# Kernel tuning notes

Hardware: AMD Instinct MI355X
Metric: run time of the kernel (lower is better)

Reference implementation:

```python
import jax, jax.numpy as jnp
import numpy as np

H = 16      # num_attention_heads
D = 64      # attention_head_size
HID = H * D # hidden_size = 1024
N = 1024    # seq_len == max_len
K = 1024    # position_buckets == att_span (K >= N so un-clamped indices stay in range)
EPS = 1e-7  # layer_norm_eps


def setup_inputs() -> dict:
    key = jax.random.key(0)
    ks = jax.random.split(key, 12)

    def w(k, shape):
        return jax.random.normal(k, shape, dtype=jnp.float32) * 0.02

    return {
        "hidden_states": jax.random.normal(ks[0], (1, N, HID), dtype=jnp.float32),
        "rel_embeddings": jax.random.normal(ks[1], (2 * K, HID), dtype=jnp.float32),
        "Wq": w(ks[2], (HID, HID)), "bq": jnp.zeros((HID,), jnp.float32),
        "Wk": w(ks[3], (HID, HID)), "bk": jnp.zeros((HID,), jnp.float32),
        "Wv": w(ks[4], (HID, HID)), "bv": jnp.zeros((HID,), jnp.float32),
        "Wpk": w(ks[5], (HID, HID)), "bpk": jnp.zeros((HID,), jnp.float32),
        "Wpq": w(ks[6], (HID, HID)), "bpq": jnp.zeros((HID,), jnp.float32),
        "Wo": w(ks[7], (HID, HID)), "bo": jnp.zeros((HID,), jnp.float32),
        "ln_g": jnp.ones((HID,), jnp.float32),
        "ln_b": jnp.zeros((HID,), jnp.float32),
    }


def _heads(x):
    # (L, HID) -> (H, L, D)   (batch size is 1, matching the baked-in id offsets)
    L = x.shape[0]
    return x.reshape(L, H, D).transpose(1, 0, 2)


def reference(hidden_states, rel_embeddings, Wq, bq, Wk, bk, Wv, bv,
              Wpk, bpk, Wpq, bpq, Wo, bo, ln_g, ln_b):
    hs = hidden_states[0]                       # (N, HID)
    q = _heads(hs @ Wq.T + bq)                  # (H, N, D)
    k = _heads(hs @ Wk.T + bk)                  # (H, N, D)
    v = _heads(hs @ Wv.T + bv)                  # (H, N, D)

    scale = jnp.sqrt(jnp.asarray(D * 3, jnp.float32))  # scale_factor = 1 + c2p + p2c = 3
    scores = jnp.einsum('hid,hjd->hij', q, k) / scale  # (H, N, N)

    pos_k = _heads(rel_embeddings @ Wpk.T + bpk)       # (H, 2K, D)
    pos_q = _heads(rel_embeddings @ Wpq.T + bpq)       # (H, 2K, D)

    rows = jnp.arange(N)[:, None]                      # (N, 1)
    # ids[i, j] = (i - j) + K  (no clamp in the original; valid since K >= N)
    idx = K + jnp.arange(N)[:, None] - jnp.arange(N)[None, :]  # (N, N)

    # c2p: gather c2p_att[h, i, K + i - j]
    c2p_att = jnp.einsum('hid,hkd->hik', q, pos_k)     # (H, N, 2K)
    c2p = c2p_att[:, rows, idx]                        # (H, N, N)

    # p2c: gather p2c_att[h, i, K + j - i], then transpose last two dims
    p2c_att = jnp.einsum('hid,hkd->hik', k, pos_q)     # (H, N, 2K)
    p2c = jnp.swapaxes(p2c_att[:, rows, idx.T], -1, -2)  # (H, N, N)

    scores = scores + (c2p + p2c) / scale
    attn = jax.nn.softmax(scores, axis=-1)             # (H, N, N)

    ctx = jnp.einsum('hij,hjd->hid', attn, v)          # (H, N, D)
    ctx = ctx.transpose(1, 0, 2).reshape(1, N, HID)    # (1, N, HID)

    # DebertaV2SelfOutput: dense + residual LayerNorm
    out = ctx @ Wo.T + bo
    x = out + hidden_states
    mu = jnp.mean(x, axis=-1, keepdims=True)
    var = jnp.mean(jnp.square(x - mu), axis=-1, keepdims=True)
    return ((x - mu) / jnp.sqrt(var + EPS)) * ln_g + ln_b
```

## Files before the change

### kernel.cpp

```cpp
#include <hip/hip_runtime.h>
#include <stdint.h>

#define HID 1024
#define NSEQ 1024
#define KREL 1024
#define NHEAD 16
#define DHEAD 64

typedef __attribute__((ext_vector_type(8))) short bhalf8;
typedef __attribute__((ext_vector_type(4))) float floatx4;

__device__ inline uint16_t f2bf(float f) {
  union { float f; uint32_t u; } c; c.f = f;
  uint32_t u = c.u;
  return (uint16_t)((u + 0x7fffu + ((u >> 16) & 1u)) >> 16);
}
__device__ inline uint32_t pkbf(float a, float b) {
  union { float f; uint32_t u; } x, y; x.f = a; y.f = b;
#if __has_builtin(__builtin_amdgcn_perm)
  return __builtin_amdgcn_perm(x.u + 0x8000u, y.u + 0x8000u, 0x03020706u);
#else
  return ((x.u + 0x8000u) >> 16) | ((y.u + 0x8000u) & 0xffff0000u);
#endif
}
__device__ inline uint32_t cvtpk(float lo, float hi) {
  uint32_t r;
  asm("v_cvt_pk_bf16_f32 %0, %1, %2" : "=v"(r) : "v"(lo), "v"(hi));
  return r;
}
__device__ inline uint4 cvt8(float4 a, float4 b) {
  uint4 r;
  r.x = cvtpk(a.x, a.y); r.y = cvtpk(a.z, a.w);
  r.z = cvtpk(b.x, b.y); r.w = cvtpk(b.z, b.w);
  return r;
}

struct ProjArgs {
  const float* A[5];
  const float* W[5];
  const float* bias[5];
  uint16_t* C[5];
  int trans[5];
};
__global__ __launch_bounds__(512) void proj_gemm(ProjArgs pa) {
  __shared__ uint16_t a_s[2][128 * 40];
  __shared__ uint16_t b_s[2][128 * 40];
  int bidx = blockIdx.x;
  int xcd = bidx & 7, idx = bidx >> 3;
  int g = xcd * 7 + (idx >> 3);
  int nt = idx & 7;
  int z, mt;
  if (g < 24) { z = g >> 3; mt = g & 7; }
  else { int g2 = g - 24; z = 3 + (g2 >> 4); mt = g2 & 15; }
  const float* A = pa.A[z];
  const float* W = pa.W[z];
  int i0 = mt * 128, n0 = nt * 128;

  int t = threadIdx.x;
  int lane = t & 63, w = t >> 6;
  int fm = lane & 15, kq = lane >> 4;
  int wm = (w >> 2) * 64, wn = (w & 3) * 32;

  int ra = t >> 2, ca = (t & 3) * 8;
  const float* Ap = A + (size_t)(i0 + ra) * HID + ca;
  const float* Wp = W + (size_t)(n0 + ra) * HID + ca;

  floatx4 acc[4][2] = {};

  float4 fa0 = *(const float4*)(Ap);
  float4 fa1 = *(const float4*)(Ap + 4);
  float4 fb0 = *(const float4*)(Wp);
  float4 fb1 = *(const float4*)(Wp + 4);
  *(uint4*)(&a_s[0][ra * 40 + ca]) = cvt8(fa0, fa1);
  *(uint4*)(&b_s[0][ra * 40 + ca]) = cvt8(fb0, fb1);

  for (int kt = 0; kt < 32; ++kt) {
    __syncthreads();
    int cur = kt & 1;
    if (kt < 31) {
      int ko = (kt + 1) * 32;
      fa0 = *(const float4*)(Ap + ko);
      fa1 = *(const float4*)(Ap + ko + 4);
      fb0 = *(const float4*)(Wp + ko);
      fb1 = *(const float4*)(Wp + ko + 4);
    }
    const uint16_t* as = &a_s[cur][0];
    const uint16_t* bs = &b_s[cur][0];
    bhalf8 af[4], bf[2];
#pragma unroll
    for (int m2 = 0; m2 < 4; ++m2)
      af[m2] = *(bhalf8*)(as + (wm + m2 * 16 + fm) * 40 + kq * 8);
#pragma unroll
    for (int n2 = 0; n2 < 2; ++n2)
      bf[n2] = *(bhalf8*)(bs + (wn + n2 * 16 + fm) * 40 + kq * 8);
#pragma unroll
    for (int m2 = 0; m2 < 4; ++m2)
#pragma unroll
      for (int n2 = 0; n2 < 2; ++n2)
        acc[m2][n2] = __builtin_amdgcn_mfma_f32_16x16x32_bf16(af[m2], bf[n2], acc[m2][n2], 0, 0, 0);
    if (kt < 31) {
      int nxt = cur ^ 1;
      *(uint4*)(&a_s[nxt][ra * 40 + ca]) = cvt8(fa0, fa1);
      *(uint4*)(&b_s[nxt][ra * 40 + ca]) = cvt8(fb0, fb1);
    }
  }

  const float* bias = pa.bias[z];
  uint16_t* C = pa.C[z];
  int tr = pa.trans[z];
#pragma unroll
  for (int m2 = 0; m2 < 4; ++m2) {
    int rowb = i0 + wm + m2 * 16 + kq * 4;
#pragma unroll
    for (int n2 = 0; n2 < 2; ++n2) {
      int col = n0 + wn + n2 * 16 + fm;
      float bv = bias[col];
      floatx4 v = acc[m2][n2];
      if (tr) {
        uint2 p = { pkbf(v[0] + bv, v[1] + bv), pkbf(v[2] + bv, v[3] + bv) };
        *(uint2*)(C + (size_t)col * NSEQ + rowb) = p;
      } else {
#pragma unroll
        for (int r = 0; r < 4; ++r)
          C[(size_t)(rowb + r) * HID + col] = f2bf(v[r] + bv);
      }
    }
  }
}

__global__ __launch_bounds__(256) void out_gemm(const uint16_t* __restrict__ Abf,
                                                const float* __restrict__ W,
                                                const float* __restrict__ bias,
                                                float* __restrict__ C) {
  __shared__ uint16_t a_s[2][64 * 40];
  __shared__ uint16_t b_s[2][64 * 40];
  int bidx = blockIdx.x;
  int i0 = (bidx >> 4) * 64, n0 = (bidx & 15) * 64;
  int t = threadIdx.x;
  int lane = t & 63, w = t >> 6;
  int fm = lane & 15, kq = lane >> 4;
  int wm = (w >> 1) * 32, wn = (w & 1) * 32;
  int ra = t >> 2, ca = (t & 3) * 8;
  const uint16_t* Ap = Abf + (size_t)(i0 + ra) * HID + ca;
  const float* Wp = W + (size_t)(n0 + ra) * HID + ca;
  floatx4 acc00 = {0,0,0,0}, acc01 = {0,0,0,0}, acc10 = {0,0,0,0}, acc11 = {0,0,0,0};
  uint4 ua = *(const uint4*)(Ap);
  float4 fw0 = *(const float4*)(Wp);
  float4 fw1 = *(const float4*)(Wp + 4);
  *(uint4*)(&a_s[0][ra * 40 + ca]) = ua;
  *(uint4*)(&b_s[0][ra * 40 + ca]) = cvt8(fw0, fw1);
  for (int kt = 0; kt < 32; ++kt) {
    __syncthreads();
    int cur = kt & 1;
    if (kt < 31) {
      int ko = (kt + 1) * 32;
      ua = *(const uint4*)(Ap + ko);
      fw0 = *(const float4*)(Wp + ko);
      fw1 = *(const float4*)(Wp + ko + 4);
    }
    const uint16_t* as = &a_s[cur][0];
    const uint16_t* bs = &b_s[cur][0];
    bhalf8 a0 = *(bhalf8*)(as + (wm + fm) * 40 + kq * 8);
    bhalf8 a1 = *(bhalf8*)(as + (wm + 16 + fm) * 40 + kq * 8);
    bhalf8 b0 = *(bhalf8*)(bs + (wn + fm) * 40 + kq * 8);
    bhalf8 b1 = *(bhalf8*)(bs + (wn + 16 + fm) * 40 + kq * 8);
    acc00 = __builtin_amdgcn_mfma_f32_16x16x32_bf16(a0, b0, acc00, 0, 0, 0);
    acc01 = __builtin_amdgcn_mfma_f32_16x16x32_bf16(a0, b1, acc01, 0, 0, 0);
    acc10 = __builtin_amdgcn_mfma_f32_16x16x32_bf16(a1, b0, acc10, 0, 0, 0);
    acc11 = __builtin_amdgcn_mfma_f32_16x16x32_bf16(a1, b1, acc11, 0, 0, 0);
    if (kt < 31) {
      int nxt = cur ^ 1;
      *(uint4*)(&a_s[nxt][ra * 40 + ca]) = ua;
      *(uint4*)(&b_s[nxt][ra * 40 + ca]) = cvt8(fw0, fw1);
    }
  }
  int rb0 = kq * 4;
#define EPO(ACC, SM, SN)                                                   \
  {                                                                        \
    int rowb = i0 + wm + (SM)*16 + rb0;                                    \
    int col = n0 + wn + (SN)*16 + fm;                                      \
    float bv_ = bias[col];                                                 \
    _Pragma("unroll")                                                      \
    for (int rr = 0; rr < 4; ++rr)                                         \
      C[(size_t)(rowb + rr) * HID + col] = ACC[rr] + bv_;                  \
  }
  EPO(acc00, 0, 0) EPO(acc01, 0, 1) EPO(acc10, 1, 0) EPO(acc11, 1, 1)
#undef EPO
}

__global__ __launch_bounds__(256) void attn_kernel(const uint16_t* __restrict__ qg,
                                                   const uint16_t* __restrict__ kg,
                                                   const uint16_t* __restrict__ vtg,
                                                   const uint16_t* __restrict__ pkg,
                                                   const uint16_t* __restrict__ pqg,
                                                   uint16_t* __restrict__ ctx) {
  const float RSCALE = 0.07216878364870323f;
  __shared__ uint16_t Qs[32][72];
  __shared__ uint16_t Ks[32][72];
  __shared__ uint16_t Vt[64][40];
  __shared__ float C2Ps[2][32][68];
  __shared__ float P2C[2][32][68];
  __shared__ float Sqk[2][32][36];
  __shared__ uint16_t Pbf[32][40];
  __shared__ float m_sm[32], l_sm[32], al_sm[32];

  int t = threadIdx.x;
  int lane = t & 63, w = t >> 6;
  int fm = lane & 15;
  int kq = lane >> 4;

  int b = blockIdx.x;
  int xcd = b & 7, slot = b >> 3;
  int h = xcd * 2 + (slot & 1);
  int i0 = (slot >> 1) * 32;
  int cb = h * DHEAD;

  {
    int r = t >> 3, chq = (t & 7) * 8;
    *(uint4*)(&Qs[r][chq]) = *(const uint4*)(qg + (size_t)(i0 + r) * HID + cb + chq);
  }
  if (t < 32) { m_sm[t] = -1e30f; l_sm[t] = 0.f; }

  floatx4 opv0 = {0,0,0,0}, opv1 = {0,0,0,0};
  int wn = w * 16;
  int smt = w >> 1, snt = w & 1;
  int i2 = t >> 3, jj4 = (t & 7) * 4;

  int pr = t >> 3, pch = (t & 7) * 8;
  int rV = t >> 2, cV = (t & 3) * 8;
  const uint16_t* kb = kg + cb + pch;
  const uint16_t* vb = vtg + (size_t)(cb + rV) * HID + cV;

  int ntb = (w & 1) * 2;
  int brow_f = ntb * 16 + fm;
  const uint16_t* bgp = ((w < 2) ? pkg : pqg) + cb + kq * 8;
  int cbase = 31 - brow_f + kq * 4;

  uint4 rk, rv;
  bhalf8 nbA0, nbA1, nbB0, nbB1;

#define STAGE1(BUF, BA0, BA1, BB0, BB1)                                          \
  do {                                                                           \
    if (w < 2) {                                                                 \
      _Pragma("unroll")                                                          \
      for (int mt = 0; mt < 2; ++mt) {                                           \
        bhalf8 a0 = *(bhalf8*)(&Qs[mt * 16 + fm][kq * 8]);                       \
        bhalf8 a1 = *(bhalf8*)(&Qs[mt * 16 + fm][kq * 8 + 32]);                  \
        floatx4 ac0 = {0,0,0,0}, ac1 = {0,0,0,0};                                \
        ac0 = __builtin_amdgcn_mfma_f32_16x16x32_bf16(a0, BA0, ac0, 0, 0, 0);    \
        ac0 = __builtin_amdgcn_mfma_f32_16x16x32_bf16(a1, BA1, ac0, 0, 0, 0);    \
        ac1 = __builtin_amdgcn_mfma_f32_16x16x32_bf16(a0, BB0, ac1, 0, 0, 0);    \
        ac1 = __builtin_amdgcn_mfma_f32_16x16x32_bf16(a1, BB1, ac1, 0, 0, 0);    \
        _Pragma("unroll")                                                        \
        for (int r = 0; r < 4; ++r) {                                            \
          int i = mt * 16 + kq * 4 + r;                                          \
          C2Ps[BUF][i][(cbase + mt * 16 + r) & 63] = ac0[r];                     \
          C2Ps[BUF][i][(cbase + mt * 16 + r - 16) & 63] = ac1[r];                \
        }                                                                        \
      }                                                                          \
    } else {                                                                     \
      _Pragma("unroll")                                                          \
      for (int mt = 0; mt < 2; ++mt) {                                           \
        bhalf8 a0 = *(bhalf8*)(&Ks[mt * 16 + fm][kq * 8]);                       \
        bhalf8 a1 = *(bhalf8*)(&Ks[mt * 16 + fm][kq * 8 + 32]);                  \
        floatx4 ac0 = {0,0,0,0}, ac1 = {0,0,0,0};                                \
        ac0 = __builtin_amdgcn_mfma_f32_16x16x32_bf16(a0, BA0, ac0, 0, 0, 0);    \
        ac0 = __builtin_amdgcn_mfma_f32_16x16x32_bf16(a1, BA1, ac0, 0, 0, 0);    \
        ac1 = __builtin_amdgcn_mfma_f32_16x16x32_bf16(a0, BB0, ac1, 0, 0, 0);    \
        ac1 = __builtin_amdgcn_mfma_f32_16x16x32_bf16(a1, BB1, ac1, 0, 0, 0);    \
        _Pragma("unroll")                                                        \
        for (int r = 0; r < 4; ++r) {                                            \
          int jr = mt * 16 + kq * 4 + r;                                         \
          P2C[BUF][jr][brow_f] = ac0[r];                                         \
          P2C[BUF][jr][brow_f + 16] = ac1[r];                                    \
        }                                                                        \
      }                                                                          \
    }                                                                            \
    {                                                                            \
      bhalf8 qa0 = *(bhalf8*)(&Qs[smt * 16 + fm][kq * 8]);                       \
      bhalf8 qa1 = *(bhalf8*)(&Qs[smt * 16 + fm][kq * 8 + 32]);                  \
      bhalf8 kb0 = *(bhalf8*)(&Ks[snt * 16 + fm][kq * 8]);                       \
      bhalf8 kb1 = *(bhalf8*)(&Ks[snt * 16 + fm][kq * 8 + 32]);                  \
      floatx4 sacc = {0,0,0,0};                                                  \
      sacc = __builtin_amdgcn_mfma_f32_16x16x32_bf16(qa0, kb0, sacc, 0, 0, 0);   \
      sacc = __builtin_amdgcn_mfma_f32_16x16x32_bf16(qa1, kb1, sacc, 0, 0, 0);   \
      _Pragma("unroll")                                                          \
      for (int r = 0; r < 4; ++r)                                                \
        Sqk[BUF][smt * 16 + kq * 4 + r][snt * 16 + fm] = sacc[r];                \
    }                                                                            \
  } while (0)

  rk = *(const uint4*)(kb);
  rv = *(const uint4*)(vb);
  *(uint4*)(&Ks[pr][pch]) = rk;
  *(uint4*)(&Vt[rV][cV]) = rv;
  __syncthreads();
  rk = *(const uint4*)(kb + (size_t)(32 + pr) * HID);
  rv = *(const uint4*)(vb + 32);
  {
    int rbase = KREL + i0 - 31;
    int r0 = rbase + brow_f;      if (r0 > 2047) r0 = 2047;
    int r1 = rbase + brow_f + 16; if (r1 > 2047) r1 = 2047;
    bhalf8 tA0 = *(const bhalf8*)(bgp + ((size_t)r0 << 10));
    bhalf8 tA1 = *(const bhalf8*)(bgp + ((size_t)r0 << 10) + 32);
    bhalf8 tB0 = *(const bhalf8*)(bgp + ((size_t)r1 << 10));
    bhalf8 tB1 = *(const bhalf8*)(bgp + ((size_t)r1 << 10) + 32);
    STAGE1(0, tA0, tA1, tB0, tB1);
  }
  __syncthreads();
  {
    *(uint4*)(&Ks[pr][pch]) = rk;
    rk = *(const uint4*)(kb + (size_t)(64 + pr) * HID);
    int rb1 = KREL + i0 - 63;
    int r0 = rb1 + brow_f;
    nbA0 = *(const bhalf8*)(bgp + ((size_t)r0 << 10));
    nbA1 = *(const bhalf8*)(bgp + ((size_t)r0 << 10) + 32);
    nbB0 = *(const bhalf8*)(bgp + ((size_t)(r0 + 16) << 10));
    nbB1 = *(const bhalf8*)(bgp + ((size_t)(r0 + 16) << 10) + 32);
  }
  __syncthreads();

  for (int jt = 0; jt < NSEQ / 32; ++jt) {
    int cur = jt & 1;

    float4 v_sqk = *(const float4*)(&Sqk[cur][i2][jj4]);
    float4 v_c2p = *(const float4*)(&C2Ps[cur][i2][jj4]);
    float p0 = P2C[cur][jj4 + 0][i2 - jj4 + 31];
    float p1 = P2C[cur][jj4 + 1][i2 - jj4 + 30];
    float p2 = P2C[cur][jj4 + 2][i2 - jj4 + 29];
    float p3 = P2C[cur][jj4 + 3][i2 - jj4 + 28];

    if (jt < 31) {
      int bi = cur ^ 1;
      STAGE1(bi, nbA0, nbA1, nbB0, nbB1);
    }

    {
      float sv0 = (v_sqk.x + v_c2p.x + p0) * RSCALE;
      float sv1 = (v_sqk.y + v_c2p.y + p1) * RSCALE;
      float sv2 = (v_sqk.z + v_c2p.z + p2) * RSCALE;
      float sv3 = (v_sqk.w + v_c2p.w + p3) * RSCALE;
      float mx = fmaxf(fmaxf(sv0, sv1), fmaxf(sv2, sv3));
      mx = fmaxf(mx, __shfl_xor(mx, 1));
      mx = fmaxf(mx, __shfl_xor(mx, 2));
      mx = fmaxf(mx, __shfl_xor(mx, 4));
      float m_old = m_sm[i2];
      float m_new = fmaxf(m_old, mx);
      float al = __expf(m_old - m_new);
      float e0 = __expf(sv0 - m_new);
      float e1 = __expf(sv1 - m_new);
      float e2 = __expf(sv2 - m_new);
      float e3 = __expf(sv3 - m_new);
      uint2 pk2v;
      pk2v.x = (uint32_t)f2bf(e0) | ((uint32_t)f2bf(e1) << 16);
      pk2v.y = (uint32_t)f2bf(e2) | ((uint32_t)f2bf(e3) << 16);
      *(uint2*)(&Pbf[i2][jj4]) = pk2v;
      float ts = (e0 + e1) + (e2 + e3);
      ts += __shfl_xor(ts, 1);
      ts += __shfl_xor(ts, 2);
      ts += __shfl_xor(ts, 4);
      if (jj4 == 0) { m_sm[i2] = m_new; l_sm[i2] = l_sm[i2] * al + ts; al_sm[i2] = al; }
    }
    __syncthreads();

    {
      floatx4 al0 = *(const floatx4*)(&al_sm[kq * 4]);
      floatx4 al1 = *(const floatx4*)(&al_sm[16 + kq * 4]);
#pragma unroll
      for (int r = 0; r < 4; ++r) {
        opv0[r] *= al0[r];
        opv1[r] *= al1[r];
      }
      bhalf8 vbf = *(bhalf8*)(&Vt[wn + fm][kq * 8]);
      bhalf8 pa0 = *(bhalf8*)(&Pbf[fm][kq * 8]);
      bhalf8 pa1 = *(bhalf8*)(&Pbf[16 + fm][kq * 8]);
      opv0 = __builtin_amdgcn_mfma_f32_16x16x32_bf16(pa0, vbf, opv0, 0, 0, 0);
      opv1 = __builtin_amdgcn_mfma_f32_16x16x32_bf16(pa1, vbf, opv1, 0, 0, 0);
      if (jt < 31) *(uint4*)(&Vt[rV][cV]) = rv;
      if (jt < 30) rv = *(const uint4*)(vb + (jt + 2) * 32);
    }
    if (jt < 30) {
      *(uint4*)(&Ks[pr][pch]) = rk;
    }
    if (jt < 29) {
      rk = *(const uint4*)(kb + (size_t)((jt + 3) * 32 + pr) * HID);
    }
    if (jt < 30) {
      int rb = KREL + i0 - (jt + 2) * 32 - 31;
      int r0 = rb + brow_f;
      nbA0 = *(const bhalf8*)(bgp + ((size_t)r0 << 10));
      nbA1 = *(const bhalf8*)(bgp + ((size_t)r0 << 10) + 32);
      nbB0 = *(const bhalf8*)(bgp + ((size_t)(r0 + 16) << 10));
      nbB1 = *(const bhalf8*)(bgp + ((size_t)(r0 + 16) << 10) + 32);
    }
    __syncthreads();
  }
#undef STAGE1

  {
    floatx4 l0 = *(const floatx4*)(&l_sm[kq * 4]);
    floatx4 l1 = *(const floatx4*)(&l_sm[16 + kq * 4]);
#pragma unroll
    for (int r = 0; r < 4; ++r) {
      int ia = kq * 4 + r, ib = 16 + kq * 4 + r;
      ctx[(size_t)(i0 + ia) * HID + cb + wn + fm] = f2bf(opv0[r] / l0[r]);
      ctx[(size_t)(i0 + ib) * HID + cb + wn + fm] = f2bf(opv1[r] / l1[r]);
    }
  }
}

__global__ __launch_bounds__(256) void ln_kernel(const float* __restrict__ xin,
                                                 const float* __restrict__ hs,
                                                 const float* __restrict__ g,
                                                 const float* __restrict__ b,
                                                 float* __restrict__ y) {
  int row = blockIdx.x, t = threadIdx.x;
  int c = t * 4;
  float4 a = *(const float4*)(xin + (size_t)row * HID + c);
  float4 hv = *(const float4*)(hs + (size_t)row * HID + c);
  float x0 = a.x + hv.x, x1 = a.y + hv.y, x2 = a.z + hv.z, x3 = a.w + hv.w;
  float s = x0 + x1 + x2 + x3;
  float sq = x0 * x0 + x1 * x1 + x2 * x2 + x3 * x3;
  for (int off = 32; off; off >>= 1) {
    s += __shfl_xor(s, off);
    sq += __shfl_xor(sq, off);
  }
  __shared__ float rs[4], rq[4];
  int w = t >> 6, lane = t & 63;
  if (lane == 0) { rs[w] = s; rq[w] = sq; }
  __syncthreads();
  s = rs[0] + rs[1] + rs[2] + rs[3];
  sq = rq[0] + rq[1] + rq[2] + rq[3];
  float mu = s * (1.0f / HID);
  float var = sq * (1.0f / HID) - mu * mu;
  float rstd = rsqrtf(var + 1e-7f);
  float4 gg = *(const float4*)(g + c);
  float4 bb = *(const float4*)(b + c);
  float4 out;
  out.x = (x0 - mu) * rstd * gg.x + bb.x;
  out.y = (x1 - mu) * rstd * gg.y + bb.y;
  out.z = (x2 - mu) * rstd * gg.z + bb.z;
  out.w = (x3 - mu) * rstd * gg.w + bb.w;
  *(float4*)(y + (size_t)row * HID + c) = out;
}

extern "C" void kernel_launch(void* const* d_in, const int* in_sizes, int n_in,
                              void* d_out, int out_size, void* d_ws, size_t ws_size,
                              hipStream_t stream) {
  const float* hs  = (const float*)d_in[0];
  const float* rel = (const float*)d_in[1];
  const float* Wq  = (const float*)d_in[2];  const float* bq  = (const float*)d_in[3];
  const float* Wk  = (const float*)d_in[4];  const float* bk  = (const float*)d_in[5];
  const float* Wv  = (const float*)d_in[6];  const float* bv  = (const float*)d_in[7];
  const float* Wpk = (const float*)d_in[8];  const float* bpk = (const float*)d_in[9];
  const float* Wpq = (const float*)d_in[10]; const float* bpq = (const float*)d_in[11];
  const float* Wo  = (const float*)d_in[12]; const float* bo  = (const float*)d_in[13];
  const float* lng = (const float*)d_in[14]; const float* lnb = (const float*)d_in[15];

  char* ws = (char*)d_ws;
  const size_t MB = 1024 * 1024;
  uint16_t* q_bf   = (uint16_t*)(ws + 0 * MB);
  uint16_t* k_bf   = (uint16_t*)(ws + 2 * MB);
  uint16_t* vt_bf  = (uint16_t*)(ws + 4 * MB);
  uint16_t* pk_bf  = (uint16_t*)(ws + 6 * MB);
  uint16_t* pq_bf  = (uint16_t*)(ws + 10 * MB);
  uint16_t* ctx_bf = (uint16_t*)(ws + 14 * MB);
  float*    out_f  = (float*)   (ws + 16 * MB);

  dim3 blk(256);

  ProjArgs pa;
  pa.A[0] = hs;  pa.A[1] = hs;  pa.A[2] = hs;  pa.A[3] = rel; pa.A[4] = rel;
  pa.W[0] = Wq;  pa.W[1] = Wk;  pa.W[2] = Wv;  pa.W[3] = Wpk; pa.W[4] = Wpq;
  pa.bias[0] = bq;  pa.bias[1] = bk;  pa.bias[2] = bv;  pa.bias[3] = bpk; pa.bias[4] = bpq;
  pa.C[0] = q_bf; pa.C[1] = k_bf; pa.C[2] = vt_bf; pa.C[3] = pk_bf; pa.C[4] = pq_bf;
  pa.trans[0] = 0; pa.trans[1] = 0; pa.trans[2] = 1; pa.trans[3] = 0; pa.trans[4] = 0;
  proj_gemm<<<dim3(448), dim3(512), 0, stream>>>(pa);

  attn_kernel<<<dim3(512), blk, 0, stream>>>(q_bf, k_bf, vt_bf, pk_bf, pq_bf, ctx_bf);

  out_gemm<<<dim3(256), blk, 0, stream>>>(ctx_bf, Wo, bo, out_f);

  ln_kernel<<<dim3(1024), blk, 0, stream>>>(out_f, hs, lng, lnb, (float*)d_out);
}
```

Before: 196.4 us.

## Fuse all stages into one persistent kernel with grid-wide atomic barriers

Replaces the four kernel launches (projection GEMM, attention, output GEMM, layernorm) with a single 512-block kernel that separates the stages with software grid barriers built on atomic counters and a shared-memory union. The projection stage is rewritten to 256 threads per block with a 64x64 per-wave tile to fit the common block size. The aim is to remove launch gaps and inter-kernel drain. The cost is spin-wait barrier overhead, occupancy limited by the largest shared-memory footprint, idle blocks in the smaller stages, and a deadlock risk if not all 512 blocks are co-resident.

Result: slower. 360.1 us (+83.4%).

```diff
diff --git a/kernel.cpp b/kernel.cpp
--- a/kernel.cpp
+++ b/kernel.cpp
@@ -42,202 +42,197 @@
   uint16_t* C[5];
   int trans[5];
 };
-__global__ __launch_bounds__(512) void proj_gemm(ProjArgs pa) {
-  __shared__ uint16_t a_s[2][128 * 40];
-  __shared__ uint16_t b_s[2][128 * 40];
+
+union SharedU {
+  struct { uint16_t a_s[2][128 * 40]; uint16_t b_s[2][128 * 40]; } proj;
+  struct { uint16_t a_s[2][64 * 40]; uint16_t b_s[2][64 * 40]; } outp;
+  struct {
+    uint16_t Qs[32][72]; uint16_t Ks[32][72]; uint16_t Vt[64][40];
+    float C2Ps[2][32][68]; float P2C[2][32][68]; float Sqk[2][32][36];
+    uint16_t Pbf[32][40]; float m_sm[32]; float l_sm[32]; float al_sm[32];
+  } attn;
+  struct { float rs[4]; float rq[4]; } ln;
+};
+
+__device__ inline void gbar(unsigned* bar) {
+  __syncthreads();
+  if (threadIdx.x == 0) {
+    __threadfence();
+    atomicAdd(bar, 1u);
+    while (atomicAdd(bar, 0u) < 512u) __builtin_amdgcn_s_sleep(4);
+    __threadfence();
+  }
+  __syncthreads();
+}
+
+__global__ __launch_bounds__(64) void init_bar(unsigned* bars) {
+  if (threadIdx.x < 4) bars[threadIdx.x] = 0u;
+}
+
+__global__ void __launch_bounds__(256) mega_kernel(ProjArgs pa,
+                                                   const float* __restrict__ Wo,
+                                                   const float* __restrict__ bo,
+                                                   const float* __restrict__ hsf,
+                                                   const float* __restrict__ lng,
+                                                   const float* __restrict__ lnb,
+                                                   float* __restrict__ dout,
+                                                   uint16_t* __restrict__ q_bf,
+                                                   uint16_t* __restrict__ k_bf,
+                                                   uint16_t* __restrict__ vt_bf,
+                                                   uint16_t* __restrict__ pk_bf,
+                                                   uint16_t* __restrict__ pq_bf,
+                                                   uint16_t* __restrict__ ctx_bf,
+                                                   float* __restrict__ out_f,
+                                                   unsigned* __restrict__ bars) {
+  __shared__ SharedU sh;
+  int t = threadIdx.x;
   int bidx = blockIdx.x;
-  int xcd = bidx & 7, idx = bidx >> 3;
-  int g = xcd * 7 + (idx >> 3);
-  int nt = idx & 7;
-  int z, mt;
-  if (g < 24) { z = g >> 3; mt = g & 7; }
-  else { int g2 = g - 24; z = 3 + (g2 >> 4); mt = g2 & 15; }
-  const float* A = pa.A[z];
-  const float* W = pa.W[z];
-  int i0 = mt * 128, n0 = nt * 128;
-
-  int t = threadIdx.x;
-  int lane = t & 63, w = t >> 6;
-  int fm = lane & 15, kq = lane >> 4;
-  int wm = (w >> 2) * 64, wn = (w & 3) * 32;
-
-  int ra = t >> 2, ca = (t & 3) * 8;
-  const float* Ap = A + (size_t)(i0 + ra) * HID + ca;
-  const float* Wp = W + (size_t)(n0 + ra) * HID + ca;
-
-  floatx4 acc[4][2] = {};
-
-  float4 fa0 = *(const float4*)(Ap);
-  float4 fa1 = *(const float4*)(Ap + 4);
-  float4 fb0 = *(const float4*)(Wp);
-  float4 fb1 = *(const float4*)(Wp + 4);
-  *(uint4*)(&a_s[0][ra * 40 + ca]) = cvt8(fa0, fa1);
-  *(uint4*)(&b_s[0][ra * 40 + ca]) = cvt8(fb0, fb1);
-
-  for (int kt = 0; kt < 32; ++kt) {
-    __syncthreads();
-    int cur = kt & 1;
-    if (kt < 31) {
-      int ko = (kt + 1) * 32;
-      fa0 = *(const float4*)(Ap + ko);
-      fa1 = *(const float4*)(Ap + ko + 4);
-      fb0 = *(const float4*)(Wp + ko);
-      fb1 = *(const float4*)(Wp + ko + 4);
-    }
-    const uint16_t* as = &a_s[cur][0];
-    const uint16_t* bs = &b_s[cur][0];
-    bhalf8 af[4], bf[2];
-#pragma unroll
-    for (int m2 = 0; m2 < 4; ++m2)
-      af[m2] = *(bhalf8*)(as + (wm + m2 * 16 + fm) * 40 + kq * 8);
-#pragma unroll
-    for (int n2 = 0; n2 < 2; ++n2)
-      bf[n2] = *(bhalf8*)(bs + (wn + n2 * 16 + fm) * 40 + kq * 8);
-#pragma unroll
-    for (int m2 = 0; m2 < 4; ++m2)
-#pragma unroll
-      for (int n2 = 0; n2 < 2; ++n2)
-        acc[m2][n2] = __builtin_amdgcn_mfma_f32_16x16x32_bf16(af[m2], bf[n2], acc[m2][n2], 0, 0, 0);
-    if (kt < 31) {
-      int nxt = cur ^ 1;
-      *(uint4*)(&a_s[nxt][ra * 40 + ca]) = cvt8(fa0, fa1);
-      *(uint4*)(&b_s[nxt][ra * 40 + ca]) = cvt8(fb0, fb1);
+
+  if (bidx < 448) {
+    uint16_t (&a_s)[2][128 * 40] = sh.proj.a_s;
+    uint16_t (&b_s)[2][128 * 40] = sh.proj.b_s;
+    int xcd = bidx & 7, idx = bidx >> 3;
+    int g = xcd * 7 + (idx >> 3);
+    int nt = idx & 7;
+    int z, mt;
+    if (g < 24) { z = g >> 3; mt = g & 7; }
+    else { int g2 = g - 24; z = 3 + (g2 >> 4); mt = g2 & 15; }
+    const float* A = pa.A[z];
+    const float* W = pa.W[z];
+    int i0 = mt * 128, n0 = nt * 128;
+
+    int lane = t & 63, w = t >> 6;
+    int fm = lane & 15, kq = lane >> 4;
+    int wm = (w >> 1) * 64, wn = (w & 1) * 64;
+
+    int ra = t >> 1, ca = (t & 1) * 16;
+    const float* Ap = A + (size_t)(i0 + ra) * HID + ca;
+    const float* Wp = W + (size_t)(n0 + ra) * HID + ca;
+
+    floatx4 acc[4][4] = {};
+
+    float4 fa[4], fb[4];
+#pragma unroll
+    for (int u = 0; u < 4; ++u) {
+      fa[u] = *(const float4*)(Ap + u * 4);
+      fb[u] = *(const float4*)(Wp + u * 4);
+    }
+    *(uint4*)(&a_s[0][ra * 40 + ca]) = cvt8(fa[0], fa[1]);
+    *(uint4*)(&a_s[0][ra * 40 + ca + 8]) = cvt8(fa[2], fa[3]);
+    *(uint4*)(&b_s[0][ra * 40 + ca]) = cvt8(fb[0], fb[1]);
+    *(uint4*)(&b_s[0][ra * 40 + ca + 8]) = cvt8(fb[2], fb[3]);
+
+    for (int kt = 0; kt < 32; ++kt) {
+      __syncthreads();
+      int cur = kt & 1;
+      if (kt < 31) {
+        int ko = (kt + 1) * 32;
+#pragma unroll
+        for (int u = 0; u < 4; ++u) {
+          fa[u] = *(const float4*)(Ap + ko + u * 4);
+          fb[u] = *(const float4*)(Wp + ko + u * 4);
+        }
+      }
+      const uint16_t* as = &a_s[cur][0];
+      const uint16_t* bs = &b_s[cur][0];
+      bhalf8 af[4], bf[4];
+#pragma unroll
+      for (int m2 = 0; m2 < 4; ++m2)
+        af[m2] = *(bhalf8*)(as + (wm + m2 * 16 + fm) * 40 + kq * 8);
+#pragma unroll
+      for (int n2 = 0; n2 < 4; ++n2)
+        bf[n2] = *(bhalf8*)(bs + (wn + n2 * 16 + fm) * 40 + kq * 8);
+#pragma unroll
+      for (int m2 = 0; m2 < 4; ++m2)
+#pragma unroll
+        for (int n2 = 0; n2 < 4; ++n2)
+          acc[m2][n2] = __builtin_amdgcn_mfma_f32_16x16x32_bf16(af[m2], bf[n2], acc[m2][n2], 0, 0, 0);
+      if (kt < 31) {
+        int nxt = cur ^ 1;
+        *(uint4*)(&a_s[nxt][ra * 40 + ca]) = cvt8(fa[0], fa[1]);
+        *(uint4*)(&a_s[nxt][ra * 40 + ca + 8]) = cvt8(fa[2], fa[3]);
+        *(uint4*)(&b_s[nxt][ra * 40 + ca]) = cvt8(fb[0], fb[1]);
+        *(uint4*)(&b_s[nxt][ra * 40 + ca + 8]) = cvt8(fb[2], fb[3]);
+      }
+    }
+
+    const float* bias = pa.bias[z];
+    uint16_t* C = pa.C[z];
+    int tr = pa.trans[z];
+#pragma unroll
+    for (int m2 = 0; m2 < 4; ++m2) {
+      int rowb = i0 + wm + m2 * 16 + kq * 4;
+#pragma unroll
+      for (int n2 = 0; n2 < 4; ++n2) {
+        int col = n0 + wn + n2 * 16 + fm;
+        float bv = bias[col];
+        floatx4 v = acc[m2][n2];
+        if (tr) {
+          uint2 p = { pkbf(v[0] + bv, v[1] + bv), pkbf(v[2] + bv, v[3] + bv) };
+          *(uint2*)(C + (size_t)col * NSEQ + rowb) = p;
+        } else {
+#pragma unroll
+          for (int r = 0; r < 4; ++r)
+            C[(size_t)(rowb + r) * HID + col] = f2bf(v[r] + bv);
+        }
+      }
     }
   }
-
-  const float* bias = pa.bias[z];
-  uint16_t* C = pa.C[z];
-  int tr = pa.trans[z];
-#pragma unroll
-  for (int m2 = 0; m2 < 4; ++m2) {
-    int rowb = i0 + wm + m2 * 16 + kq * 4;
-#pragma unroll
-    for (int n2 = 0; n2 < 2; ++n2) {
-      int col = n0 + wn + n2 * 16 + fm;
-      float bv = bias[col];
-      floatx4 v = acc[m2][n2];
-      if (tr) {
-        uint2 p = { pkbf(v[0] + bv, v[1] + bv), pkbf(v[2] + bv, v[3] + bv) };
-        *(uint2*)(C + (size_t)col * NSEQ + rowb) = p;
-      } else {
-#pragma unroll
-        for (int r = 0; r < 4; ++r)
-          C[(size_t)(rowb + r) * HID + col] = f2bf(v[r] + bv);
-      }
-    }
-  }
-}
-
-__global__ __launch_bounds__(256) void out_gemm(const uint16_t* __restrict__ Abf,
-                                                const float* __restrict__ W,
-                                                const float* __restrict__ bias,
-                                                float* __restrict__ C) {
-  __shared__ uint16_t a_s[2][64 * 40];
-  __shared__ uint16_t b_s[2][64 * 40];
-  int bidx = blockIdx.x;
-  int i0 = (bidx >> 4) * 64, n0 = (bidx & 15) * 64;
-  int t = threadIdx.x;
-  int lane = t & 63, w = t >> 6;
-  int fm = lane & 15, kq = lane >> 4;
-  int wm = (w >> 1) * 32, wn = (w & 1) * 32;
-  int ra = t >> 2, ca = (t & 3) * 8;
-  const uint16_t* Ap = Abf + (size_t)(i0 + ra) * HID + ca;
-  const float* Wp = W + (size_t)(n0 + ra) * HID + ca;
-  floatx4 acc00 = {0,0,0,0}, acc01 = {0,0,0,0}, acc10 = {0,0,0,0}, acc11 = {0,0,0,0};
-  uint4 ua = *(const uint4*)(Ap);
-  float4 fw0 = *(const float4*)(Wp);
-  float4 fw1 = *(const float4*)(Wp + 4);
-  *(uint4*)(&a_s[0][ra * 40 + ca]) = ua;
-  *(uint4*)(&b_s[0][ra * 40 + ca]) = cvt8(fw0, fw1);
-  for (int kt = 0; kt < 32; ++kt) {
-    __syncthreads();
-    int cur = kt & 1;
-    if (kt < 31) {
-      int ko = (kt + 1) * 32;
-      ua = *(const uint4*)(Ap + ko);
-      fw0 = *(const float4*)(Wp + ko);
-      fw1 = *(const float4*)(Wp + ko + 4);
-    }
-    const uint16_t* as = &a_s[cur][0];
-    const uint16_t* bs = &b_s[cur][0];
-    bhalf8 a0 = *(bhalf8*)(as + (wm + fm) * 40 + kq * 8);
-    bhalf8 a1 = *(bhalf8*)(as + (wm + 16 + fm) * 40 + kq * 8);
-    bhalf8 b0 = *(bhalf8*)(bs + (wn + fm) * 40 + kq * 8);
-    bhalf8 b1 = *(bhalf8*)(bs + (wn + 16 + fm) * 40 + kq * 8);
-    acc00 = __builtin_amdgcn_mfma_f32_16x16x32_bf16(a0, b0, acc00, 0, 0, 0);
-    acc01 = __builtin_amdgcn_mfma_f32_16x16x32_bf16(a0, b1, acc01, 0, 0, 0);
-    acc10 = __builtin_amdgcn_mfma_f32_16x16x32_bf16(a1, b0, acc10, 0, 0, 0);
-    acc11 = __builtin_amdgcn_mfma_f32_16x16x32_bf16(a1, b1, acc11, 0, 0, 0);
-    if (kt < 31) {
-      int nxt = cur ^ 1;
-      *(uint4*)(&a_s[nxt][ra * 40 + ca]) = ua;
-      *(uint4*)(&b_s[nxt][ra * 40 + ca]) = cvt8(fw0, fw1);
-    }
-  }
-  int rb0 = kq * 4;
-#define EPO(ACC, SM, SN)                                                   \
-  {                                                                        \
-    int rowb = i0 + wm + (SM)*16 + rb0;                                    \
-    int col = n0 + wn + (SN)*16 + fm;                                      \
-    float bv_ = bias[col];                                                 \
-    _Pragma("unroll")                                                      \
-    for (int rr = 0; rr < 4; ++rr)                                         \
-      C[(size_t)(rowb + rr) * HID + col] = ACC[rr] + bv_;                  \
-  }
-  EPO(acc00, 0, 0) EPO(acc01, 0, 1) EPO(acc10, 1, 0) EPO(acc11, 1, 1)
-#undef EPO
-}
-
-__global__ __launch_bounds__(256) void attn_kernel(const uint16_t* __restrict__ qg,
-                                                   const uint16_t* __restrict__ kg,
-                                                   const uint16_t* __restrict__ vtg,
-                                                   const uint16_t* __restrict__ pkg,
-                                                   const uint16_t* __restrict__ pqg,
-                                                   uint16_t* __restrict__ ctx) {
-  const float RSCALE = 0.07216878364870323f;
-  __shared__ uint16_t Qs[32][72];
-  __shared__ uint16_t Ks[32][72];
-  __shared__ uint16_t Vt[64][40];
-  __shared__ float C2Ps[2][32][68];
-  __shared__ float P2C[2][32][68];
-  __shared__ float Sqk[2][32][36];
-  __shared__ uint16_t Pbf[32][40];
-  __shared__ float m_sm[32], l_sm[32], al_sm[32];
-
-  int t = threadIdx.x;
-  int lane = t & 63, w = t >> 6;
-  int fm = lane & 15;
-  int kq = lane >> 4;
-
-  int b = blockIdx.x;
-  int xcd = b & 7, slot = b >> 3;
-  int h = xcd * 2 + (slot & 1);
-  int i0 = (slot >> 1) * 32;
-  int cb = h * DHEAD;
+  gbar(&bars[0]);
 
   {
-    int r = t >> 3, chq = (t & 7) * 8;
-    *(uint4*)(&Qs[r][chq]) = *(const uint4*)(qg + (size_t)(i0 + r) * HID + cb + chq);
-  }
-  if (t < 32) { m_sm[t] = -1e30f; l_sm[t] = 0.f; }
-
-  floatx4 opv0 = {0,0,0,0}, opv1 = {0,0,0,0};
-  int wn = w * 16;
-  int smt = w >> 1, snt = w & 1;
-  int i2 = t >> 3, jj4 = (t & 7) * 4;
-
-  int pr = t >> 3, pch = (t & 7) * 8;
-  int rV = t >> 2, cV = (t & 3) * 8;
-  const uint16_t* kb = kg + cb + pch;
-  const uint16_t* vb = vtg + (size_t)(cb + rV) * HID + cV;
-
-  int ntb = (w & 1) * 2;
-  int brow_f = ntb * 16 + fm;
-  const uint16_t* bgp = ((w < 2) ? pkg : pqg) + cb + kq * 8;
-  int cbase = 31 - brow_f + kq * 4;
-
-  uint4 rk, rv;
-  bhalf8 nbA0, nbA1, nbB0, nbB1;
+    const float RSCALE = 0.07216878364870323f;
+    uint16_t (&Qs)[32][72] = sh.attn.Qs;
+    uint16_t (&Ks)[32][72] = sh.attn.Ks;
+    uint16_t (&Vt)[64][40] = sh.attn.Vt;
+    float (&C2Ps)[2][32][68] = sh.attn.C2Ps;
+    float (&P2C)[2][32][68] = sh.attn.P2C;
+    float (&Sqk)[2][32][36] = sh.attn.Sqk;
+    uint16_t (&Pbf)[32][40] = sh.attn.Pbf;
+    float (&m_sm)[32] = sh.attn.m_sm;
+    float (&l_sm)[32] = sh.attn.l_sm;
+    float (&al_sm)[32] = sh.attn.al_sm;
+
+    const uint16_t* qg = q_bf;
+    const uint16_t* kg = k_bf;
+    const uint16_t* vtg = vt_bf;
+    const uint16_t* pkg = pk_bf;
+    const uint16_t* pqg = pq_bf;
+    uint16_t* ctx = ctx_bf;
+
+    int lane = t & 63, w = t >> 6;
+    int fm = lane & 15;
+    int kq = lane >> 4;
+
+    int b = bidx;
+    int xcd = b & 7, slot = b >> 3;
+    int h = xcd * 2 + (slot & 1);
+    int i0 = (slot >> 1) * 32;
+    int cb = h * DHEAD;
+
+    {
+      int r = t >> 3, chq = (t & 7) * 8;
+      *(uint4*)(&Qs[r][chq]) = *(const uint4*)(qg + (size_t)(i0 + r) * HID + cb + chq);
+    }
+    if (t < 32) { m_sm[t] = -1e30f; l_sm[t] = 0.f; }
+
+    floatx4 opv0 = {0,0,0,0}, opv1 = {0,0,0,0};
+    int wn = w * 16;
+    int smt = w >> 1, snt = w & 1;
+    int i2 = t >> 3, jj4 = (t & 7) * 4;
+
+    int pr = t >> 3, pch = (t & 7) * 8;
+    int rV = t >> 2, cV = (t & 3) * 8;
+    const uint16_t* kb = kg + cb + pch;
+    const uint16_t* vb = vtg + (size_t)(cb + rV) * HID + cV;
+
+    int ntb = (w & 1) * 2;
+    int brow_f = ntb * 16 + fm;
+    const uint16_t* bgp = ((w < 2) ? pkg : pqg) + cb + kq * 8;
+    int cbase = 31 - brow_f + kq * 4;
+
+    uint4 rk, rv;
+    bhalf8 nbA0, nbA1, nbB0, nbB1;
 
 #define STAGE1(BUF, BA0, BA1, BB0, BB1)                                          \
   do {                                                                           \
@@ -290,158 +285,217 @@
     }                                                                            \
   } while (0)
 
-  rk = *(const uint4*)(kb);
-  rv = *(const uint4*)(vb);
-  *(uint4*)(&Ks[pr][pch]) = rk;
-  *(uint4*)(&Vt[rV][cV]) = rv;
-  __syncthreads();
-  rk = *(const uint4*)(kb + (size_t)(32 + pr) * HID);
-  rv = *(const uint4*)(vb + 32);
-  {
-    int rbase = KREL + i0 - 31;
-    int r0 = rbase + brow_f;      if (r0 > 2047) r0 = 2047;
-    int r1 = rbase + brow_f + 16; if (r1 > 2047) r1 = 2047;
-    bhalf8 tA0 = *(const bhalf8*)(bgp + ((size_t)r0 << 10));
-    bhalf8 tA1 = *(const bhalf8*)(bgp + ((size_t)r0 << 10) + 32);
-    bhalf8 tB0 = *(const bhalf8*)(bgp + ((size_t)r1 << 10));
-    bhalf8 tB1 = *(const bhalf8*)(bgp + ((size_t)r1 << 10) + 32);
-    STAGE1(0, tA0, tA1, tB0, tB1);
-  }
-  __syncthreads();
-  {
+    rk = *(const uint4*)(kb);
+    rv = *(const uint4*)(vb);
     *(uint4*)(&Ks[pr][pch]) = rk;
-    rk = *(const uint4*)(kb + (size_t)(64 + pr) * HID);
-    int rb1 = KREL + i0 - 63;
-    int r0 = rb1 + brow_f;
-    nbA0 = *(const bhalf8*)(bgp + ((size_t)r0 << 10));
-    nbA1 = *(const bhalf8*)(bgp + ((size_t)r0 << 10) + 32);
-    nbB0 = *(const bhalf8*)(bgp + ((size_t)(r0 + 16) << 10));
-    nbB1 = *(const bhalf8*)(bgp + ((size_t)(r0 + 16) << 10) + 32);
-  }
-  __syncthreads();
-
-  for (int jt = 0; jt < NSEQ / 32; ++jt) {
-    int cur = jt & 1;
-
-    float4 v_sqk = *(const float4*)(&Sqk[cur][i2][jj4]);
-    float4 v_c2p = *(const float4*)(&C2Ps[cur][i2][jj4]);
-    float p0 = P2C[cur][jj4 + 0][i2 - jj4 + 31];
-    float p1 = P2C[cur][jj4 + 1][i2 - jj4 + 30];
-    float p2 = P2C[cur][jj4 + 2][i2 - jj4 + 29];
-    float p3 = P2C[cur][jj4 + 3][i2 - jj4 + 28];
-
-    if (jt < 31) {
-      int bi = cur ^ 1;
-      STAGE1(bi, nbA0, nbA1, nbB0, nbB1);
-    }
-
+    *(uint4*)(&Vt[rV][cV]) = rv;
+    __syncthreads();
+    rk = *(const uint4*)(kb + (size_t)(32 + pr) * HID);
+    rv = *(const uint4*)(vb + 32);
     {
-      float sv0 = (v_sqk.x + v_c2p.x + p0) * RSCALE;
-      float sv1 = (v_sqk.y + v_c2p.y + p1) * RSCALE;
-      float sv2 = (v_sqk.z + v_c2p.z + p2) * RSCALE;
-      float sv3 = (v_sqk.w + v_c2p.w + p3) * RSCALE;
-      float mx = fmaxf(fmaxf(sv0, sv1), fmaxf(sv2, sv3));
-      mx = fmaxf(mx, __shfl_xor(mx, 1));
-      mx = fmaxf(mx, __shfl_xor(mx, 2));
-      mx = fmaxf(mx, __shfl_xor(mx, 4));
-      float m_old = m_sm[i2];
-      float m_new = fmaxf(m_old, mx);
-      float al = __expf(m_old - m_new);
-      float e0 = __expf(sv0 - m_new);
-      float e1 = __expf(sv1 - m_new);
-      float e2 = __expf(sv2 - m_new);
-      float e3 = __expf(sv3 - m_new);
-      uint2 pk2v;
-      pk2v.x = (uint32_t)f2bf(e0) | ((uint32_t)f2bf(e1) << 16);
-      pk2v.y = (uint32_t)f2bf(e2) | ((uint32_t)f2bf(e3) << 16);
-      *(uint2*)(&Pbf[i2][jj4]) = pk2v;
-      float ts = (e0 + e1) + (e2 + e3);
-      ts += __shfl_xor(ts, 1);
-      ts += __shfl_xor(ts, 2);
-      ts += __shfl_xor(ts, 4);
-      if (jj4 == 0) { m_sm[i2] = m_new; l_sm[i2] = l_sm[i2] * al + ts; al_sm[i2] = al; }
+      int rbase = KREL + i0 - 31;
+      int r0 = rbase + brow_f;      if (r0 > 2047) r0 = 2047;
+      int r1 = rbase + brow_f + 16; if (r1 > 2047) r1 = 2047;
+      bhalf8 tA0 = *(const bhalf8*)(bgp + ((size_t)r0 << 10));
+      bhalf8 tA1 = *(const bhalf8*)(bgp + ((size_t)r0 << 10) + 32);
+      bhalf8 tB0 = *(const bhalf8*)(bgp + ((size_t)r1 << 10));
+      bhalf8 tB1 = *(const bhalf8*)(bgp + ((size_t)r1 << 10) + 32);
+      STAGE1(0, tA0, tA1, tB0, tB1);
     }
     __syncthreads();
-
     {
-      floatx4 al0 = *(const floatx4*)(&al_sm[kq * 4]);
-      floatx4 al1 = *(const floatx4*)(&al_sm[16 + kq * 4]);
-#pragma unroll
-      for (int r = 0; r < 4; ++r) {
-        opv0[r] *= al0[r];
-        opv1[r] *= al1[r];
-      }
-      bhalf8 vbf = *(bhalf8*)(&Vt[wn + fm][kq * 8]);
-      bhalf8 pa0 = *(bhalf8*)(&Pbf[fm][kq * 8]);
-      bhalf8 pa1 = *(bhalf8*)(&Pbf[16 + fm][kq * 8]);
-      opv0 = __builtin_amdgcn_mfma_f32_16x16x32_bf16(pa0, vbf, opv0, 0, 0, 0);
-      opv1 = __builtin_amdgcn_mfma_f32_16x16x32_bf16(pa1, vbf, opv1, 0, 0, 0);
-      if (jt < 31) *(uint4*)(&Vt[rV][cV]) = rv;
-      if (jt < 30) rv = *(const uint4*)(vb + (jt + 2) * 32);
-    }
-    if (jt < 30) {
       *(uint4*)(&Ks[pr][pch]) = rk;
-    }
-    if (jt < 29) {
-      rk = *(const uint4*)(kb + (size_t)((jt + 3) * 32 + pr) * HID);
-    }
-    if (jt < 30) {
-      int rb = KREL + i0 - (jt + 2) * 32 - 31;
-      int r0 = rb + brow_f;
+      rk = *(const uint4*)(kb + (size_t)(64 + pr) * HID);
+      int rb1 = KREL + i0 - 63;
+      int r0 = rb1 + brow_f;
       nbA0 = *(const bhalf8*)(bgp + ((size_t)r0 << 10));
       nbA1 = *(const bhalf8*)(bgp + ((size_t)r0 << 10) + 32);
       nbB0 = *(const bhalf8*)(bgp + ((size_t)(r0 + 16) << 10));
       nbB1 = *(const bhalf8*)(bgp + ((size_t)(r0 + 16) << 10) + 32);
     }
     __syncthreads();
+
+    for (int jt = 0; jt < NSEQ / 32; ++jt) {
+      int cur = jt & 1;
+
+      float4 v_sqk = *(const float4*)(&Sqk[cur][i2][jj4]);
+      float4 v_c2p = *(const float4*)(&C2Ps[cur][i2][jj4]);
+      float p0 = P2C[cur][jj4 + 0][i2 - jj4 + 31];
+      float p1 = P2C[cur][jj4 + 1][i2 - jj4 + 30];
+      float p2 = P2C[cur][jj4 + 2][i2 - jj4 + 29];
+      float p3 = P2C[cur][jj4 + 3][i2 - jj4 + 28];
+
+      if (jt < 31) {
+        int bi = cur ^ 1;
+        STAGE1(bi, nbA0, nbA1, nbB0, nbB1);
+      }
+
+      {
+        float sv0 = (v_sqk.x + v_c2p.x + p0) * RSCALE;
+        float sv1 = (v_sqk.y + v_c2p.y + p1) * RSCALE;
+        float sv2 = (v_sqk.z + v_c2p.z + p2) * RSCALE;
+        float sv3 = (v_sqk.w + v_c2p.w + p3) * RSCALE;
+        float mx = fmaxf(fmaxf(sv0, sv1), fmaxf(sv2, sv3));
+        mx = fmaxf(mx, __shfl_xor(mx, 1));
+        mx = fmaxf(mx, __shfl_xor(mx, 2));
+        mx = fmaxf(mx, __shfl_xor(mx, 4));
+        float m_old = m_sm[i2];
+        float m_new = fmaxf(m_old, mx);
+        float al = __expf(m_old - m_new);
+        float e0 = __expf(sv0 - m_new);
+        float e1 = __expf(sv1 - m_new);
+        float e2 = __expf(sv2 - m_new);
+        float e3 = __expf(sv3 - m_new);
+        uint2 pk2v;
+        pk2v.x = (uint32_t)f2bf(e0) | ((uint32_t)f2bf(e1) << 16);
+        pk2v.y = (uint32_t)f2bf(e2) | ((uint32_t)f2bf(e3) << 16);
+        *(uint2*)(&Pbf[i2][jj4]) = pk2v;
+        float ts = (e0 + e1) + (e2 + e3);
+        ts += __shfl_xor(ts, 1);
+        ts += __shfl_xor(ts, 2);
+        ts += __shfl_xor(ts, 4);
+        if (jj4 == 0) { m_sm[i2] = m_new; l_sm[i2] = l_sm[i2] * al + ts; al_sm[i2] = al; }
+      }
+      __syncthreads();
+
+      {
+        floatx4 al0 = *(const floatx4*)(&al_sm[kq * 4]);
+        floatx4 al1 = *(const floatx4*)(&al_sm[16 + kq * 4]);
+#pragma unroll
+        for (int r = 0; r < 4; ++r) {
+          opv0[r] *= al0[r];
+          opv1[r] *= al1[r];
+        }
+        bhalf8 vbf = *(bhalf8*)(&Vt[wn + fm][kq * 8]);
+        bhalf8 pa0 = *(bhalf8*)(&Pbf[fm][kq * 8]);
+        bhalf8 pa1 = *(bhalf8*)(&Pbf[16 + fm][kq * 8]);
+        opv0 = __builtin_amdgcn_mfma_f32_16x16x32_bf16(pa0, vbf, opv0, 0, 0, 0);
+        opv1 = __builtin_amdgcn_mfma_f32_16x16x32_bf16(pa1, vbf, opv1, 0, 0, 0);
+        if (jt < 31) *(uint4*)(&Vt[rV][cV]) = rv;
+        if (jt < 30) rv = *(const uint4*)(vb + (jt + 2) * 32);
+      }
+      if (jt < 30) {
+        *(uint4*)(&Ks[pr][pch]) = rk;
+      }
+      if (jt < 29) {
+        rk = *(const uint4*)(kb + (size_t)((jt + 3) * 32 + pr) * HID);
+      }
+      if (jt < 30) {
+        int rb = KREL + i0 - (jt + 2) * 32 - 31;
+        int r0 = rb + brow_f;
+        nbA0 = *(const bhalf8*)(bgp + ((size_t)r0 << 10));
+        nbA1 = *(const bhalf8*)(bgp + ((size_t)r0 << 10) + 32);
+        nbB0 = *(const bhalf8*)(bgp + ((size_t)(r0 + 16) << 10));
+        nbB1 = *(const bhalf8*)(bgp + ((size_t)(r0 + 16) << 10) + 32);
+      }
+      __syncthreads();
+    }
+#undef STAGE1
+
+    {
+      floatx4 l0 = *(const floatx4*)(&l_sm[kq * 4]);
+      floatx4 l1 = *(const floatx4*)(&l_sm[16 + kq * 4]);
+#pragma unroll
+      for (int r = 0; r < 4; ++r) {
+        int ia = kq * 4 + r, ib = 16 + kq * 4 + r;
+        ctx[(size_t)(i0 + ia) * HID + cb + wn + fm] = f2bf(opv0[r] / l0[r]);
+        ctx[(size_t)(i0 + ib) * HID + cb + wn + fm] = f2bf(opv1[r] / l1[r]);
+      }
+    }
   }
-#undef STAGE1
+  gbar(&bars[1]);
+
+  if (bidx < 256) {
+    uint16_t (&a_s)[2][64 * 40] = sh.outp.a_s;
+    uint16_t (&b_s)[2][64 * 40] = sh.outp.b_s;
+    int i0 = (bidx >> 4) * 64, n0 = (bidx & 15) * 64;
+    int lane = t & 63, w = t >> 6;
+    int fm = lane & 15, kq = lane >> 4;
+    int wm = (w >> 1) * 32, wn = (w & 1) * 32;
+    int ra = t >> 2, ca = (t & 3) * 8;
+    const uint16_t* Ap = ctx_bf + (size_t)(i0 + ra) * HID + ca;
+    const float* Wp = Wo + (size_t)(n0 + ra) * HID + ca;
+    floatx4 acc00 = {0,0,0,0}, acc01 = {0,0,0,0}, acc10 = {0,0,0,0}, acc11 = {0,0,0,0};
+    uint4 ua = *(const uint4*)(Ap);
+    float4 fw0 = *(const float4*)(Wp);
+    float4 fw1 = *(const float4*)(Wp + 4);
+    *(uint4*)(&a_s[0][ra * 40 + ca]) = ua;
+    *(uint4*)(&b_s[0][ra * 40 + ca]) = cvt8(fw0, fw1);
+    for (int kt = 0; kt < 32; ++kt) {
+      __syncthreads();
+      int cur = kt & 1;
+      if (kt < 31) {
+        int ko = (kt + 1) * 32;
+        ua = *(const uint4*)(Ap + ko);
+        fw0 = *(const float4*)(Wp + ko);
+        fw1 = *(const float4*)(Wp + ko + 4);
+      }
+      const uint16_t* as = &a_s[cur][0];
+      const uint16_t* bs = &b_s[cur][0];
+      bhalf8 a0 = *(bhalf8*)(as + (wm + fm) * 40 + kq * 8);
+      bhalf8 a1 = *(bhalf8*)(as + (wm + 16 + fm) * 40 + kq * 8);
+      bhalf8 b0 = *(bhalf8*)(bs + (wn + fm) * 40 + kq * 8);
+      bhalf8 b1 = *(bhalf8*)(bs + (wn + 16 + fm) * 40 + kq * 8);
+      acc00 = __builtin_amdgcn_mfma_f32_16x16x32_bf16(a0, b0, acc00, 0, 0, 0);
+      acc01 = __builtin_amdgcn_mfma_f32_16x16x32_bf16(a0, b1, acc01, 0, 0, 0);
+      acc10 = __builtin_amdgcn_mfma_f32_16x16x32_bf16(a1, b0, acc10, 0, 0, 0);
+      acc11 = __builtin_amdgcn_mfma_f32_16x16x32_bf16(a1, b1, acc11, 0, 0, 0);
+      if (kt < 31) {
+        int nxt = cur ^ 1;
+        *(uint4*)(&a_s[nxt][ra * 40 + ca]) = ua;
+        *(uint4*)(&b_s[nxt][ra * 40 + ca]) = cvt8(fw0, fw1);
+      }
+    }
+    int rb0 = kq * 4;
+#define EPO(ACC, SM, SN)                                                   \
+    {                                                                      \
+      int rowb = i0 + wm + (SM)*16 + rb0;                                  \
+      int col = n0 + wn + (SN)*16 + fm;                                    \
+      float bv_ = bo[col];                                                 \
+      _Pragma("unroll")                                                    \
+      for (int rr = 0; rr < 4; ++rr)                                       \
+        out_f[(size_t)(rowb + rr) * HID + col] = ACC[rr] + bv_;            \
+    }
+    EPO(acc00, 0, 0) EPO(acc01, 0, 1) EPO(acc10, 1, 0) EPO(acc11, 1, 1)
+#undef EPO
+  }
+  gbar(&bars[2]);
 
   {
-    floatx4 l0 = *(const floatx4*)(&l_sm[kq * 4]);
-    floatx4 l1 = *(const floatx4*)(&l_sm[16 + kq * 4]);
-#pragma unroll
-    for (int r = 0; r < 4; ++r) {
-      int ia = kq * 4 + r, ib = 16 + kq * 4 + r;
-      ctx[(size_t)(i0 + ia) * HID + cb + wn + fm] = f2bf(opv0[r] / l0[r]);
-      ctx[(size_t)(i0 + ib) * HID + cb + wn + fm] = f2bf(opv1[r] / l1[r]);
+    float (&rs)[4] = sh.ln.rs;
+    float (&rq)[4] = sh.ln.rq;
+    int w = t >> 6, lane = t & 63;
+    int c = t * 4;
+    float4 gg = *(const float4*)(lng + c);
+    float4 bb = *(const float4*)(lnb + c);
+#pragma unroll
+    for (int rr2 = 0; rr2 < 2; ++rr2) {
+      int row = bidx * 2 + rr2;
+      float4 a = *(const float4*)(out_f + (size_t)row * HID + c);
+      float4 hv = *(const float4*)(hsf + (size_t)row * HID + c);
+      float x0 = a.x + hv.x, x1 = a.y + hv.y, x2 = a.z + hv.z, x3 = a.w + hv.w;
+      float s = x0 + x1 + x2 + x3;
+      float sq = x0 * x0 + x1 * x1 + x2 * x2 + x3 * x3;
+      for (int off = 32; off; off >>= 1) {
+        s += __shfl_xor(s, off);
+        sq += __shfl_xor(sq, off);
+      }
+      __syncthreads();
+      if (lane == 0) { rs[w] = s; rq[w] = sq; }
+      __syncthreads();
+      s = rs[0] + rs[1] + rs[2] + rs[3];
+      sq = rq[0] + rq[1] + rq[2] + rq[3];
+      float mu = s * (1.0f / HID);
+      float var = sq * (1.0f / HID) - mu * mu;
+      float rstd = rsqrtf(var + 1e-7f);
+      float4 out;
+      out.x = (x0 - mu) * rstd * gg.x + bb.x;
+      out.y = (x1 - mu) * rstd * gg.y + bb.y;
+      out.z = (x2 - mu) * rstd * gg.z + bb.z;
+      out.w = (x3 - mu) * rstd * gg.w + bb.w;
+      *(float4*)(dout + (size_t)row * HID + c) = out;
     }
   }
-}
-
-__global__ __launch_bounds__(256) void ln_kernel(const float* __restrict__ xin,
-                                                 const float* __restrict__ hs,
-                                                 const float* __restrict__ g,
-                                                 const float* __restrict__ b,
-                                                 float* __restrict__ y) {
-  int row = blockIdx.x, t = threadIdx.x;
-  int c = t * 4;
-  float4 a = *(const float4*)(xin + (size_t)row * HID + c);
-  float4 hv = *(const float4*)(hs + (size_t)row * HID + c);
-  float x0 = a.x + hv.x, x1 = a.y + hv.y, x2 = a.z + hv.z, x3 = a.w + hv.w;
-  float s = x0 + x1 + x2 + x3;
-  float sq = x0 * x0 + x1 * x1 + x2 * x2 + x3 * x3;
-  for (int off = 32; off; off >>= 1) {
-    s += __shfl_xor(s, off);
-    sq += __shfl_xor(sq, off);
-  }
-  __shared__ float rs[4], rq[4];
-  int w = t >> 6, lane = t & 63;
-  if (lane == 0) { rs[w] = s; rq[w] = sq; }
-  __syncthreads();
-  s = rs[0] + rs[1] + rs[2] + rs[3];
-  sq = rq[0] + rq[1] + rq[2] + rq[3];
-  float mu = s * (1.0f / HID);
-  float var = sq * (1.0f / HID) - mu * mu;
-  float rstd = rsqrtf(var + 1e-7f);
-  float4 gg = *(const float4*)(g + c);
-  float4 bb = *(const float4*)(b + c);
-  float4 out;
-  out.x = (x0 - mu) * rstd * gg.x + bb.x;
-  out.y = (x1 - mu) * rstd * gg.y + bb.y;
-  out.z = (x2 - mu) * rstd * gg.z + bb.z;
-  out.w = (x3 - mu) * rstd * gg.w + bb.w;
-  *(float4*)(y + (size_t)row * HID + c) = out;
 }
 
 extern "C" void kernel_launch(void* const* d_in, const int* in_sizes, int n_in,
@@ -466,8 +520,7 @@
   uint16_t* pq_bf  = (uint16_t*)(ws + 10 * MB);
   uint16_t* ctx_bf = (uint16_t*)(ws + 14 * MB);
   float*    out_f  = (float*)   (ws + 16 * MB);
-
-  dim3 blk(256);
+  unsigned* bars   = (unsigned*)(ws + 20 * MB);
 
   ProjArgs pa;
   pa.A[0] = hs;  pa.A[1] = hs;  pa.A[2] = hs;  pa.A[3] = rel; pa.A[4] = rel;
@@ -475,11 +528,9 @@
   pa.bias[0] = bq;  pa.bias[1] = bk;  pa.bias[2] = bv;  pa.bias[3] = bpk; pa.bias[4] = bpq;
   pa.C[0] = q_bf; pa.C[1] = k_bf; pa.C[2] = vt_bf; pa.C[3] = pk_bf; pa.C[4] = pq_bf;
   pa.trans[0] = 0; pa.trans[1] = 0; pa.trans[2] = 1; pa.trans[3] = 0; pa.trans[4] = 0;
-  proj_gemm<<<dim3(448), dim3(512), 0, stream>>>(pa);
-
-  attn_kernel<<<dim3(512), blk, 0, stream>>>(q_bf, k_bf, vt_bf, pk_bf, pq_bf, ctx_bf);
-
-  out_gemm<<<dim3(256), blk, 0, stream>>>(ctx_bf, Wo, bo, out_f);
-
-  ln_kernel<<<dim3(1024), blk, 0, stream>>>(out_f, hs, lng, lnb, (float*)d_out);
-}
+
+  init_bar<<<dim3(1), dim3(64), 0, stream>>>(bars);
+  mega_kernel<<<dim3(512), dim3(256), 0, stream>>>(pa, Wo, bo, hs, lng, lnb, (float*)d_out,
+                                                   q_bf, k_bf, vt_bf, pk_bf, pq_bf, ctx_bf,
+                                                   out_f, bars);
+}
```
